# Kernel optimization log

Hardware: AMD Instinct MI355X
Metric: run time of the kernel (lower is better)

The kernel has to match this reference:

```python
import jax, jax.numpy as jnp
import numpy as np

H = 256; M = 32; IN_DIM = 131; OUT_DIM = 131; B = 32; T_IN = 129; T_OUT = 128


def setup_inputs():
    key = jax.random.key(0)
    ks = jax.random.split(key, 16)
    rn = lambda k, s, sc=0.1: (jax.random.normal(k, s) * sc).astype(jnp.float32)
    return {
        'X': rn(ks[0], (T_IN, B, IN_DIM), 1.0),
        'Y': rn(ks[1], (T_OUT, B, IN_DIM), 1.0),
        'Wih_e': rn(ks[2], (4 * H, IN_DIM + M)), 'Whh_e': rn(ks[3], (4 * H, H)),
        'bih_e': jnp.zeros(4 * H, jnp.float32), 'bhh_e': jnp.zeros(4 * H, jnp.float32),
        'Wih_d': rn(ks[4], (4 * H, IN_DIM + M)), 'Whh_d': rn(ks[5], (4 * H, H)),
        'bih_d': jnp.zeros(4 * H, jnp.float32), 'bhh_d': jnp.zeros(4 * H, jnp.float32),
        'Wd': rn(ks[6], (H,)), 'bd': jnp.zeros((), jnp.float32),
        'Wu': rn(ks[7], (H,)), 'bu': jnp.zeros((), jnp.float32),
        'Wv': rn(ks[8], (M, H)), 'bv': jnp.zeros(M, jnp.float32),
        'Wo': rn(ks[9], (H, H)), 'bo': jnp.zeros(H, jnp.float32),
        'Wlin': rn(ks[10], (OUT_DIM, H)), 'blin': jnp.zeros(OUT_DIM, jnp.float32),
        'h0': rn(ks[11], (H,), 1.0), 'c0': rn(ks[12], (H,), 1.0),
    }


def _lstm(x, h, c, Wih, Whh, bih, bhh):
    # torch.nn.LSTMCell gate order: i, f, g, o
    g = x @ Wih.T + bih + h @ Whh.T + bhh
    i, f, gg, o = jnp.split(g, 4, axis=-1)
    c = jax.nn.sigmoid(f) * c + jax.nn.sigmoid(i) * jnp.tanh(gg)
    return jax.nn.sigmoid(o) * jnp.tanh(c), c


def _suffix_excl(x):
    # out[i] = sum_{j > i} x[j]  (the O(t^2) torch loops fused to O(t) cumsum)
    return jnp.cumsum(x[::-1], axis=0)[::-1] - x


def _stack_step(Vbuf, sbuf, cnt, d, u, v):
    # Vbuf: (L,B,M) values, sbuf: (L,B) strengths, cnt valid entries, push v with strength d, pop u
    Vbuf = Vbuf.at[cnt].set(v)
    mask = (jnp.arange(Vbuf.shape[0]) < cnt)[:, None]
    s_m = jnp.where(mask, sbuf, 0.0)
    totprev = _suffix_excl(s_m)                                  # sum of strengths above i
    sn = jnp.where(mask, jax.nn.relu(s_m - jax.nn.relu(u[None, :] - totprev)), 0.0)
    sn = sn.at[cnt].set(d)
    tots = _suffix_excl(sn)
    coeff = jnp.minimum(sn, jax.nn.relu(1.0 - tots))             # (L,B); zero beyond cnt
    r = jnp.einsum('lb,lbm->bm', coeff, Vbuf)
    return Vbuf, sn, r


def reference(X, Y, Wih_e, Whh_e, bih_e, bhh_e, Wih_d, Whh_d, bih_d, bhh_d,
              Wd, bd, Wu, bu, Wv, bv, Wo, bo, Wlin, blin, h0, c0):
    Bb = X.shape[1]
    m = Wv.shape[0]
    cap = 1 + (X.shape[0] - 1) + Y.shape[0]                      # stack capacity
    h = jnp.broadcast_to(h0, (Bb, h0.shape[0]))
    c = jnp.broadcast_to(c0, (Bb, c0.shape[0]))
    Vbuf = jnp.zeros((cap, Bb, m), X.dtype)
    sbuf = jnp.zeros((cap, Bb), X.dtype)
    r = jnp.zeros((Bb, m), X.dtype)

    def ctrl(h):
        d = jax.nn.sigmoid(h @ Wd + bd)
        u = jax.nn.sigmoid(h @ Wu + bu)
        v = jnp.tanh(h @ Wv.T + bv)
        return d, u, v

    def make_step(Wih, Whh, bih, bhh, emit):
        def step(carry, x_t):
            h, c, Vbuf, sbuf, cnt, r = carry
            h, c = _lstm(jnp.concatenate([x_t, r], -1), h, c, Wih, Whh, bih, bhh)
            d, u, v = ctrl(h)
            Vbuf, sbuf, r = _stack_step(Vbuf, sbuf, cnt, d, u, v)
            out = None
            if emit:
                oc = jnp.tanh(h @ Wo.T + bo)
                out = jax.nn.log_softmax(oc @ Wlin.T + blin, axis=-1)
            return (h, c, Vbuf, sbuf, cnt + 1, r), out
        return step

    carry = (h, c, Vbuf, sbuf, jnp.int32(1), r)
    carry, _ = jax.lax.scan(make_step(Wih_e, Whh_e, bih_e, bhh_e, False), carry, X[:-1])
    dec_in = jnp.concatenate([X[-1:], Y[:-1]], axis=0)           # teacher forcing
    _, Ypred = jax.lax.scan(make_step(Wih_d, Whh_d, bih_d, bhh_d, True), carry, dec_in)
    return Ypred
```

## Files before the change

kernel.cpp:

```cpp
#include <hip/hip_runtime.h>
#include <math.h>

typedef unsigned long long u64;

namespace {
constexpr int kH    = 256;
constexpr int kM    = 32;
constexpr int kIn   = 131;
constexpr int kOut  = 131;
constexpr int kB    = 32;
constexpr int kTenc = 128;
constexpr int kT    = 256;
constexpr int kCap  = 257;
constexpr int kG    = 1024;
constexpr int kK    = 288;
constexpr int kSp   = 8;
constexpr int kSl   = 32;
constexpr int kKq   = 72;
constexpr int kWR   = 72;
constexpr int kVs   = 36;
}

__device__ __forceinline__ float frcp(float x){ return __builtin_amdgcn_rcpf(x); }
__device__ __forceinline__ float sigf(float x){ return frcp(1.0f + __expf(-x)); }
__device__ __forceinline__ float tanhf_fast(float x){
  return 1.0f - 2.0f*frcp(__expf(2.0f*x) + 1.0f);
}

template<int PAT>
__device__ __forceinline__ float swz(float x){
  return __int_as_float(__builtin_amdgcn_ds_swizzle(__float_as_int(x), PAT));
}

__global__ void k_transpose(float* __restrict__ dst, const float* __restrict__ src,
                            int R, int C, int stride, int col0){
  int idx = blockIdx.x*256 + threadIdx.x;
  if (idx >= R*C) return;
  int rr = idx / C;
  int cc = idx - rr*C;
  dst[cc*R + rr] = src[rr*stride + col0 + cc];
}

__global__ void k_packw(float* __restrict__ dst, const float* __restrict__ Wih,
                        const float* __restrict__ Whh){
  int idx = blockIdx.x*256 + threadIdx.x;
  if (idx >= kSp*kWR*512) return;
  int tid  = idx & 511;
  int rest = idx >> 9;
  int sp = rest / kWR, i = rest - sp*kWR;
  int lc = tid & 127, q = tid >> 7;
  int col = (lc >> 5)*256 + sp*kSl + (lc & 31);
  int k   = q*kKq + i;
  dst[idx] = (k < kH) ? Whh[col*kH + k] : Wih[col*(kIn+kM) + kIn + (k - kH)];
}

__global__ void k_gatesx(const float* __restrict__ X, const float* __restrict__ Y,
                         const float* __restrict__ WixT_e, const float* __restrict__ WixT_d,
                         const float* __restrict__ bih_e, const float* __restrict__ bhh_e,
                         const float* __restrict__ bih_d, const float* __restrict__ bhh_d,
                         float* __restrict__ gatesXp){
  const int t   = blockIdx.x;
  const int col = blockIdx.y*256 + threadIdx.x;
  __shared__ float xl[kB*kIn];
  const float* xsrc;
  if (t < kTenc)       xsrc = X + (size_t)t*kB*kIn;
  else if (t == kTenc) xsrc = X + (size_t)kTenc*kB*kIn;
  else                 xsrc = Y + (size_t)(t-kTenc-1)*kB*kIn;
  for (int i = threadIdx.x; i < kB*kIn; i += 256) xl[i] = xsrc[i];
  __syncthreads();
  const float* WT   = (t < kTenc) ? WixT_e : WixT_d;
  const float  bias = (t < kTenc) ? (bih_e[col] + bhh_e[col]) : (bih_d[col] + bhh_d[col]);
  float acc[kB];
#pragma unroll
  for (int b = 0; b < kB; ++b) acc[b] = bias;
  for (int k = 0; k < kIn; ++k){
    float wk = WT[k*kG + col];
#pragma unroll
    for (int b = 0; b < kB; ++b) acc[b] += wk * xl[b*kIn + k];
  }
  const int j = col & 255, g = col >> 8;
#pragma unroll
  for (int b = 0; b < kB; ++b)
    gatesXp[(((size_t)t*kB + b)*256 + j)*4 + g] = acc[b];
}

__device__ __forceinline__ float wave_suffix_incl(float x, int lane){
#pragma unroll
  for (int off = 1; off < 64; off <<= 1){
    float t = __shfl_down(x, off);
    if (lane + off < 64) x += t;
  }
  return x;
}

__global__ void __launch_bounds__(512, 1)
k_seq(const float* __restrict__ gatesXp, const float* __restrict__ wblob,
      u64* __restrict__ hbuf,
      const float* __restrict__ Wd, const float* __restrict__ bd,
      const float* __restrict__ Wu, const float* __restrict__ bu,
      const float* __restrict__ Wv, const float* __restrict__ bv,
      const float* __restrict__ h0, const float* __restrict__ c0,
      float* __restrict__ Hdec){
  const int bid  = blockIdx.x;
  const int b    = bid >> 3;
  const int sp   = bid & 7;
  const int tid  = threadIdx.x;
  const int lane = tid & 63;
  const int wave = tid >> 6;
  const int lc   = tid & 127;
  const int q    = tid >> 7;

  __shared__ __align__(16) float z[kK];
  __shared__ float cst[kSl];
  __shared__ float red[512];
  __shared__ float sbuf[kCap];
  __shared__ float coeff[kCap];
  __shared__ float Vbuf[kCap*kVs];

  if (tid < kH) z[tid] = h0[tid];
  if (tid >= kH && tid < kK) z[tid] = 0.f;
  if (tid < kSl) cst[tid] = c0[sp*kSl + tid];
  for (int i = tid; i < kCap; i += 512) sbuf[i] = 0.f;
  if (tid < kVs) Vbuf[tid] = 0.f;
  __syncthreads();

  float wreg[kWR];
  {
    const float* wb = wblob + ((size_t)sp*kWR)*512 + tid;
#pragma unroll
    for (int i = 0; i < kWR; ++i) wreg[i] = wb[(size_t)i*512];
#pragma unroll
    for (int i = 0; i < kWR; ++i) asm volatile("" : "+v"(wreg[i]));
  }

  for (int t = 0; t < kT; ++t){
    float4 gx = {0.f,0.f,0.f,0.f};
    if (tid < kSl)
      gx = *(const float4*)(gatesXp + (((size_t)t*kB + b)*256 + sp*kSl + tid)*4);

    {
      float a0=0.f,a1=0.f,a2=0.f,a3=0.f;
      const float4* z4 = (const float4*)z + q*(kKq/4);
#pragma unroll
      for (int c = 0; c < kKq/4; ++c){
        float4 zz = z4[c];
        a0 += wreg[4*c+0]*zz.x; a1 += wreg[4*c+1]*zz.y;
        a2 += wreg[4*c+2]*zz.z; a3 += wreg[4*c+3]*zz.w;
      }
      red[tid] = (a0+a1)+(a2+a3);
    }
    __syncthreads();

    if (tid < kSl){
      float gi = gx.x + ((red[tid      ] + red[tid+128+  0]) + (red[tid+256+  0] + red[tid+384+  0]));
      float gf = gx.y + ((red[ 32+tid] + red[160+tid]) + (red[288+tid] + red[416+tid]));
      float gg = gx.z + ((red[ 64+tid] + red[192+tid]) + (red[320+tid] + red[448+tid]));
      float go = gx.w + ((red[ 96+tid] + red[224+tid]) + (red[352+tid] + red[480+tid]));
      float ig = sigf(gi), fg = sigf(gf), g2 = tanhf_fast(gg), og = sigf(go);
      float cn = fg*cst[tid] + ig*g2;
      cst[tid] = cn;
      float hn = og*tanhf_fast(cn);
      const int j = sp*kSl + tid;
      z[j] = hn;
      u64 pk = ((u64)(unsigned)t << 32) | (u64)__float_as_uint(hn);
      __hip_atomic_store(hbuf + ((size_t)(t & 1)*kB + b)*kH + j, pk,
                         __ATOMIC_RELAXED, __HIP_MEMORY_SCOPE_AGENT);
      if (t >= kTenc)
        Hdec[(((size_t)(t - kTenc))*kB + b)*kH + j] = hn;
    }
    if (t == kT - 1) break;

    if (t + 1 == kTenc){
      const float* wb = wblob + ((size_t)(kSp + sp)*kWR)*512 + tid;
#pragma unroll
      for (int i = 0; i < kWR; ++i) wreg[i] = wb[(size_t)i*512];
#pragma unroll
      for (int i = 0; i < kWR; ++i) asm volatile("" : "+v"(wreg[i]));
    }

    if (tid < (kSp-1)*kSl){
      int p  = tid >> 5;
      int sp2 = p + (p >= sp);
      int j  = sp2*kSl + (tid & 31);
      const u64* src = hbuf + ((size_t)(t & 1)*kB + b)*kH + j;
      u64 v;
      do {
        v = __hip_atomic_load(src, __ATOMIC_RELAXED, __HIP_MEMORY_SCOPE_AGENT);
      } while ((unsigned)(v >> 32) != (unsigned)t);
      z[j] = __uint_as_float((unsigned)v);
    }
    __syncthreads();

    const int cnt = t + 1;
    if (wave == 0){
      const float* Wdu = (lane < 32) ? Wd : Wu;
      const int kl = lane & 31;
      float p = 0.f;
#pragma unroll
      for (int q2 = 0; q2 < 8; ++q2) p += z[kl + 32*q2] * Wdu[kl + 32*q2];
      p += swz<0x401F>(p); p += swz<0x201F>(p); p += swz<0x101F>(p);
      p += swz<0x081F>(p); p += swz<0x041F>(p);
      float o  = __shfl_xor(p, 32);
      float dd = sigf(((lane < 32) ? p : o) + bd[0]);
      float uu = sigf(((lane < 32) ? o : p) + bu[0]);

      float sm[5], sn[5];
      float csum = 0.f;
#pragma unroll
      for (int qq = 0; qq < 5; ++qq){
        int i = lane*5 + qq;
        float sv = (i < cnt) ? sbuf[i] : 0.f;
        sm[qq] = sv; csum += sv;
      }
      float run = wave_suffix_incl(csum, lane) - csum;
      float csum2 = 0.f;
#pragma unroll
      for (int qq = 4; qq >= 0; --qq){
        int i = lane*5 + qq;
        float sv;
        if (i == cnt)      sv = dd;
        else if (i < cnt)  sv = fmaxf(sm[qq] - fmaxf(uu - run, 0.f), 0.f);
        else               sv = 0.f;
        sn[qq] = sv;
        run  += sm[qq];
        csum2 += sv;
      }
#pragma unroll
      for (int qq = 0; qq < 5; ++qq){
        int i = lane*5 + qq;
        if (i < kCap) sbuf[i] = sn[qq];
      }
      float run2 = wave_suffix_incl(csum2, lane) - csum2;
#pragma unroll
      for (int qq = 4; qq >= 0; --qq){
        int i = lane*5 + qq;
        float cf = fminf(sn[qq], fmaxf(1.f - run2, 0.f));
        if (i < kCap) coeff[i] = cf;
        run2 += sn[qq];
      }
    } else if (tid >= 256){
      const int m = (tid - 256) >> 3, l = tid & 7;
      float p = 0.f;
      for (int k2 = l; k2 < kH; k2 += 8) p += z[k2] * Wv[m*kH + k2];
      p += swz<0x101F>(p); p += swz<0x081F>(p); p += swz<0x041F>(p);
      if (l == 0) Vbuf[cnt*kVs + m] = tanhf_fast(p + bv[m]);
    }
    __syncthreads();

    if (tid < kH){
      const int m = tid >> 3, l = tid & 7;
      float p = 0.f;
      for (int i = l; i <= cnt; i += 8) p += coeff[i]*Vbuf[i*kVs + m];
      p += swz<0x101F>(p); p += swz<0x081F>(p); p += swz<0x041F>(p);
      if (l == 0) z[kH + m] = p;
    }
    __syncthreads();
  }
}

__global__ void k_out(const float* __restrict__ Hdec,
                      const float* __restrict__ WoT, const float* __restrict__ bo,
                      const float* __restrict__ WlinT, const float* __restrict__ blin,
                      float* __restrict__ out){
  const int row = blockIdx.x;
  const int tid = threadIdx.x;
  __shared__ float hr[kH], oc[kH], lg[kOut], st[2];
  hr[tid] = Hdec[(size_t)row*kH + tid];
  __syncthreads();
  float a = bo[tid];
  for (int k = 0; k < kH; ++k) a += hr[k]*WoT[k*kH + tid];
  oc[tid] = tanhf(a);
  __syncthreads();
  if (tid < kOut){
    float a2 = blin[tid];
    for (int k = 0; k < kH; ++k) a2 += oc[k]*WlinT[k*kOut + tid];
    lg[tid] = a2;
  }
  __syncthreads();
  if (tid < 64){
    float mx = -3.4e38f;
    for (int i = tid; i < kOut; i += 64) mx = fmaxf(mx, lg[i]);
#pragma unroll
    for (int off = 32; off; off >>= 1) mx = fmaxf(mx, __shfl_down(mx, off));
    mx = __shfl(mx, 0);
    float se = 0.f;
    for (int i = tid; i < kOut; i += 64) se += expf(lg[i] - mx);
#pragma unroll
    for (int off = 32; off; off >>= 1) se += __shfl_down(se, off);
    if (tid == 0){ st[0] = mx; st[1] = logf(se); }
  }
  __syncthreads();
  if (tid < kOut) out[(size_t)row*kOut + tid] = lg[tid] - st[0] - st[1];
}

extern "C" void kernel_launch(void* const* d_in, const int* in_sizes, int n_in,
                              void* d_out, int out_size, void* d_ws, size_t ws_size,
                              hipStream_t stream){
  (void)in_sizes; (void)n_in; (void)out_size; (void)ws_size;
  const float* X     = (const float*)d_in[0];
  const float* Y     = (const float*)d_in[1];
  const float* Wih_e = (const float*)d_in[2];
  const float* Whh_e = (const float*)d_in[3];
  const float* bih_e = (const float*)d_in[4];
  const float* bhh_e = (const float*)d_in[5];
  const float* Wih_d = (const float*)d_in[6];
  const float* Whh_d = (const float*)d_in[7];
  const float* bih_d = (const float*)d_in[8];
  const float* bhh_d = (const float*)d_in[9];
  const float* Wd    = (const float*)d_in[10];
  const float* bd    = (const float*)d_in[11];
  const float* Wu    = (const float*)d_in[12];
  const float* bu    = (const float*)d_in[13];
  const float* Wv    = (const float*)d_in[14];
  const float* bv    = (const float*)d_in[15];
  const float* Wo    = (const float*)d_in[16];
  const float* bo    = (const float*)d_in[17];
  const float* Wlin  = (const float*)d_in[18];
  const float* blin  = (const float*)d_in[19];
  const float* h0    = (const float*)d_in[20];
  const float* c0    = (const float*)d_in[21];
  float* out = (float*)d_out;

  float* ws = (float*)d_ws;
  size_t o = 0;
  float* gatesXp = ws + o; o += (size_t)kT*kB*kG;
  float* WixT_e  = ws + o; o += (size_t)kIn*kG;
  float* WixT_d  = ws + o; o += (size_t)kIn*kG;
  float* WoT     = ws + o; o += (size_t)kH*kH;
  float* WlinT   = ws + o; o += (size_t)kH*kOut;
  float* Hdec    = ws + o; o += (size_t)128*kB*kH;
  float* wblob   = ws + o; o += (size_t)2*kSp*kWR*512;
  u64*   hbuf    = (u64*)(ws + o); o += (size_t)2*2*kB*kH;

  auto tr = [&](float* dst, const float* src, int R, int C, int stride, int col0){
    int n = R*C;
    k_transpose<<<(n+255)/256, 256, 0, stream>>>(dst, src, R, C, stride, col0);
  };
  tr(WixT_e, Wih_e, kG, kIn, kIn+kM, 0);
  tr(WixT_d, Wih_d, kG, kIn, kIn+kM, 0);
  tr(WoT,   Wo,   kH,  kH, kH, 0);
  tr(WlinT, Wlin, kOut, kH, kH, 0);

  const int npack = kSp*kWR*512;
  k_packw<<<(npack+255)/256, 256, 0, stream>>>(wblob,                 Wih_e, Whh_e);
  k_packw<<<(npack+255)/256, 256, 0, stream>>>(wblob + (size_t)npack, Wih_d, Whh_d);

  k_gatesx<<<dim3(kT,4), 256, 0, stream>>>(X, Y, WixT_e, WixT_d,
                                           bih_e, bhh_e, bih_d, bhh_d, gatesXp);
  k_seq<<<kB*kSp, 512, 0, stream>>>(gatesXp, wblob, hbuf,
                                    Wd, bd, Wu, bu, Wv, bv, h0, c0, Hdec);
  k_out<<<128*kB, 256, 0, stream>>>(Hdec, WoT, bo, WlinT, blin, out);
}
```

Baseline: 1.750 ms.

## Reduce gate sums with wave shuffles and stage stack weights in LDS

Repacks the recurrent weights so the four K-partials and four gates of one hidden unit sit in 16 adjacent lanes. The gate reduction then uses cross-lane shuffles instead of a shared-memory buffer plus a barrier. Wv, Wd, Wu and bv are copied into LDS once (Wv transposed and padded), so the per-step controller dot products stop reading global memory. The stack readout is moved to a different set of threads with 4-way splitting, and the polling threads are moved to the upper lanes. The cost is more LDS use and redundant gate math across 16 lanes.

New measurement: 1.740 ms. No clear change (-0.6%).

```diff
diff --git a/kernel.cpp b/kernel.cpp
--- a/kernel.cpp
+++ b/kernel.cpp
@@ -13,12 +13,11 @@
 constexpr int kT    = 256;
 constexpr int kCap  = 257;
 constexpr int kG    = 1024;
-constexpr int kK    = 288;
 constexpr int kSp   = 8;
 constexpr int kSl   = 32;
-constexpr int kKq   = 72;
 constexpr int kWR   = 72;
 constexpr int kVs   = 36;
+constexpr int kWvS  = 33;
 }
 
 __device__ __forceinline__ float frcp(float x){ return __builtin_amdgcn_rcpf(x); }
@@ -48,9 +47,9 @@
   int tid  = idx & 511;
   int rest = idx >> 9;
   int sp = rest / kWR, i = rest - sp*kWR;
-  int lc = tid & 127, q = tid >> 7;
-  int col = (lc >> 5)*256 + sp*kSl + (lc & 31);
-  int k   = q*kKq + i;
+  int uj = tid >> 4, g = (tid >> 2) & 3, q = tid & 3;
+  int col = g*256 + sp*kSl + uj;
+  int k   = (i < 64) ? (q*64 + i) : (256 + q*8 + (i - 64));
   dst[idx] = (k < kH) ? Whh[col*kH + k] : Wih[col*(kIn+kM) + kIn + (k - kH)];
 }
 
@@ -107,21 +106,29 @@
   const int tid  = threadIdx.x;
   const int lane = tid & 63;
   const int wave = tid >> 6;
-  const int lc   = tid & 127;
-  const int q    = tid >> 7;
-
-  __shared__ __align__(16) float z[kK];
+  const int uj   = tid >> 4;
+  const int g    = (tid >> 2) & 3;
+  const int q    = tid & 3;
+
+  __shared__ __align__(16) float z[kH + kM];
   __shared__ float cst[kSl];
-  __shared__ float red[512];
   __shared__ float sbuf[kCap];
   __shared__ float coeff[kCap];
   __shared__ float Vbuf[kCap*kVs];
+  __shared__ float WvL[kH*kWvS];
+  __shared__ float WdL[kH], WuL[kH], bvL[kM];
 
   if (tid < kH) z[tid] = h0[tid];
-  if (tid >= kH && tid < kK) z[tid] = 0.f;
+  if (tid >= kH && tid < kH+kM) z[tid] = 0.f;
   if (tid < kSl) cst[tid] = c0[sp*kSl + tid];
   for (int i = tid; i < kCap; i += 512) sbuf[i] = 0.f;
   if (tid < kVs) Vbuf[tid] = 0.f;
+  for (int i = tid; i < kH*kM; i += 512){
+    int k = i >> 5, m = i & 31;
+    WvL[k*kWvS + m] = Wv[m*kH + k];
+  }
+  if (tid < kH){ WdL[tid] = Wd[tid]; WuL[tid] = Wu[tid]; }
+  if (tid < kM) bvL[tid] = bv[tid];
   __syncthreads();
 
   float wreg[kWR];
@@ -134,36 +141,46 @@
   }
 
   for (int t = 0; t < kT; ++t){
-    float4 gx = {0.f,0.f,0.f,0.f};
-    if (tid < kSl)
-      gx = *(const float4*)(gatesXp + (((size_t)t*kB + b)*256 + sp*kSl + tid)*4);
-
+    const float4 gx = *(const float4*)(gatesXp + (((size_t)t*kB + b)*256 + sp*kSl + uj)*4);
+
+    float acc;
     {
       float a0=0.f,a1=0.f,a2=0.f,a3=0.f;
-      const float4* z4 = (const float4*)z + q*(kKq/4);
-#pragma unroll
-      for (int c = 0; c < kKq/4; ++c){
-        float4 zz = z4[c];
+      const float4* z4 = (const float4*)z;
+#pragma unroll
+      for (int c = 0; c < 16; ++c){
+        float4 zz = z4[q*16 + c];
         a0 += wreg[4*c+0]*zz.x; a1 += wreg[4*c+1]*zz.y;
         a2 += wreg[4*c+2]*zz.z; a3 += wreg[4*c+3]*zz.w;
       }
-      red[tid] = (a0+a1)+(a2+a3);
-    }
-    __syncthreads();
-
-    if (tid < kSl){
-      float gi = gx.x + ((red[tid      ] + red[tid+128+  0]) + (red[tid+256+  0] + red[tid+384+  0]));
-      float gf = gx.y + ((red[ 32+tid] + red[160+tid]) + (red[288+tid] + red[416+tid]));
-      float gg = gx.z + ((red[ 64+tid] + red[192+tid]) + (red[320+tid] + red[448+tid]));
-      float go = gx.w + ((red[ 96+tid] + red[224+tid]) + (red[352+tid] + red[480+tid]));
-      float ig = sigf(gi), fg = sigf(gf), g2 = tanhf_fast(gg), og = sigf(go);
-      float cn = fg*cst[tid] + ig*g2;
-      cst[tid] = cn;
-      float hn = og*tanhf_fast(cn);
-      const int j = sp*kSl + tid;
+      float4 t0 = z4[64 + 2*q], t1 = z4[64 + 2*q + 1];
+      a0 += wreg[64]*t0.x + wreg[68]*t1.x;
+      a1 += wreg[65]*t0.y + wreg[69]*t1.y;
+      a2 += wreg[66]*t0.z + wreg[70]*t1.z;
+      a3 += wreg[67]*t0.w + wreg[71]*t1.w;
+      acc = (a0+a1)+(a2+a3);
+    }
+    acc += __shfl_xor(acc, 1);
+    acc += __shfl_xor(acc, 2);
+    float s4  = __shfl_xor(acc, 4);
+    float s8  = __shfl_xor(acc, 8);
+    float s12 = __shfl_xor(acc, 12);
+    float gi = (g==0)?acc:(g==1)?s4:(g==2)?s8:s12;
+    float gf = (g==1)?acc:(g==0)?s4:(g==3)?s8:s12;
+    float gg = (g==2)?acc:(g==3)?s4:(g==0)?s8:s12;
+    float go = (g==3)?acc:(g==2)?s4:(g==1)?s8:s12;
+    gi += gx.x; gf += gx.y; gg += gx.z; go += gx.w;
+
+    float cold = cst[uj];
+    float ig = sigf(gi), fg = sigf(gf), g2 = tanhf_fast(gg), og = sigf(go);
+    float cn = fg*cold + ig*g2;
+    float hn = og*tanhf_fast(cn);
+    const int j = sp*kSl + uj;
+    if ((tid & 15) == 0){
+      cst[uj] = cn;
       z[j] = hn;
-      u64 pk = ((u64)(unsigned)t << 32) | (u64)__float_as_uint(hn);
-      __hip_atomic_store(hbuf + ((size_t)(t & 1)*kB + b)*kH + j, pk,
+      __hip_atomic_store(hbuf + ((size_t)(t & 1)*kB + b)*kH + j,
+                         ((u64)(unsigned)t << 32) | (u64)__float_as_uint(hn),
                          __ATOMIC_RELAXED, __HIP_MEMORY_SCOPE_AGENT);
       if (t >= kTenc)
         Hdec[(((size_t)(t - kTenc))*kB + b)*kH + j] = hn;
@@ -178,26 +195,27 @@
       for (int i = 0; i < kWR; ++i) asm volatile("" : "+v"(wreg[i]));
     }
 
-    if (tid < (kSp-1)*kSl){
-      int p  = tid >> 5;
+    if (tid >= 288){
+      int idx = tid - 288;
+      int p   = idx >> 5;
       int sp2 = p + (p >= sp);
-      int j  = sp2*kSl + (tid & 31);
-      const u64* src = hbuf + ((size_t)(t & 1)*kB + b)*kH + j;
+      int jj  = sp2*kSl + (idx & 31);
+      const u64* src = hbuf + ((size_t)(t & 1)*kB + b)*kH + jj;
       u64 v;
       do {
         v = __hip_atomic_load(src, __ATOMIC_RELAXED, __HIP_MEMORY_SCOPE_AGENT);
       } while ((unsigned)(v >> 32) != (unsigned)t);
-      z[j] = __uint_as_float((unsigned)v);
+      z[jj] = __uint_as_float((unsigned)v);
     }
     __syncthreads();
 
     const int cnt = t + 1;
     if (wave == 0){
-      const float* Wdu = (lane < 32) ? Wd : Wu;
+      const float* WduL = (lane < 32) ? WdL : WuL;
       const int kl = lane & 31;
       float p = 0.f;
 #pragma unroll
-      for (int q2 = 0; q2 < 8; ++q2) p += z[kl + 32*q2] * Wdu[kl + 32*q2];
+      for (int s = 0; s < 8; ++s) p += z[kl + 32*s] * WduL[kl + 32*s];
       p += swz<0x401F>(p); p += swz<0x201F>(p); p += swz<0x101F>(p);
       p += swz<0x081F>(p); p += swz<0x041F>(p);
       float o  = __shfl_xor(p, 32);
@@ -241,17 +259,17 @@
     } else if (tid >= 256){
       const int m = (tid - 256) >> 3, l = tid & 7;
       float p = 0.f;
-      for (int k2 = l; k2 < kH; k2 += 8) p += z[k2] * Wv[m*kH + k2];
+      for (int k2 = l; k2 < kH; k2 += 8) p += z[k2] * WvL[k2*kWvS + m];
       p += swz<0x101F>(p); p += swz<0x081F>(p); p += swz<0x041F>(p);
-      if (l == 0) Vbuf[cnt*kVs + m] = tanhf_fast(p + bv[m]);
+      if (l == 0) Vbuf[cnt*kVs + m] = tanhf_fast(p + bvL[m]);
     }
     __syncthreads();
 
-    if (tid < kH){
-      const int m = tid >> 3, l = tid & 7;
+    if (tid >= 64 && tid < 192){
+      const int m = (tid - 64) >> 2, l = tid & 3;
       float p = 0.f;
-      for (int i = l; i <= cnt; i += 8) p += coeff[i]*Vbuf[i*kVs + m];
-      p += swz<0x101F>(p); p += swz<0x081F>(p); p += swz<0x041F>(p);
+      for (int i = l; i <= cnt; i += 4) p += coeff[i]*Vbuf[i*kVs + m];
+      p += swz<0x041F>(p); p += swz<0x081F>(p);
       if (l == 0) z[kH + m] = p;
     }
     __syncthreads();
```
